# Kernel tuning notes

Measured on AMD Instinct MI355X. Metric: run time of the kernel, lower is better.

The kernel has to match this reference:

```python
import jax, jax.numpy as jnp
import numpy as np

GROUPS = 32
EPS = 1e-3  # keras GroupNormalization default epsilon


def setup_inputs() -> dict:
    key = jax.random.key(0)
    ks = jax.random.split(key, 7)
    B, H, W, C = 16, 32, 32, 512
    inputs = jax.random.normal(ks[0], (B, H, W, C), dtype=jnp.float32)
    gamma = jnp.ones((C,), dtype=jnp.float32)
    beta = jnp.zeros((C,), dtype=jnp.float32)
    # EinsumDense 'bhwc,cae->bhwae', output last dims (C,3), bias axes 'ae'
    W_qkv = jax.random.normal(ks[1], (C, C, 3), dtype=jnp.float32) / np.sqrt(C)
    b_qkv = jnp.zeros((C, 3), dtype=jnp.float32)
    # EinsumDense 'bhwc,cd->bhwd', bias axes 'd'
    W_out = jax.random.normal(ks[2], (C, C), dtype=jnp.float32) / np.sqrt(C)
    b_out = jnp.zeros((C,), dtype=jnp.float32)
    return {
        "inputs": inputs,
        "gamma": gamma,
        "beta": beta,
        "W_qkv": W_qkv,
        "b_qkv": b_qkv,
        "W_out": W_out,
        "b_out": b_out,
    }


def group_norm(x, gamma, beta):
    B, H, W, C = x.shape
    g = GROUPS
    xr = x.reshape(B, H, W, g, C // g)
    mean = jnp.mean(xr, axis=(1, 2, 4), keepdims=True)
    var = jnp.var(xr, axis=(1, 2, 4), keepdims=True)
    xn = (xr - mean) * jax.lax.rsqrt(var + EPS)
    return xn.reshape(B, H, W, C) * gamma + beta


def reference(inputs, gamma, beta, W_qkv, b_qkv, W_out, b_out):
    B, H, W, C = inputs.shape
    scale = C ** (-0.5)
    x = group_norm(inputs, gamma, beta)
    # QKV projection: bhwc,cae->bhwae  (+ bias over 'ae')
    qkv = jnp.einsum("bhwc,cae->bhwae", x, W_qkv) + b_qkv
    q, k, v = qkv[..., 0], qkv[..., 1], qkv[..., 2]  # each [B,H,W,C]
    # full spatial attention: [B,H,W,H,W]
    attn = jnp.einsum("bhwc,btlc->bhwtl", q, k) * scale
    attn = attn.reshape(B, H, W, H * W)
    attn = jax.nn.softmax(attn, axis=-1)
    attn = attn.reshape(B, H, W, H, W)
    out = jnp.einsum("bhwtl,btlc->bhwc", attn, v)
    out = jnp.einsum("bhwc,cd->bhwd", out, W_out) + b_out
    return inputs + out
```

## Files before the change

kernel.cpp:

```cpp
#include <hip/hip_runtime.h>
#include <hip/hip_bf16.h>

#define NB    16
#define SP    1024
#define NC    512
#define NG    32
#define MTOT  (NB*SP)
#define EPSV  1e-3f
#define SCALE 0.04419417382415922f

using f32x4   = __attribute__((ext_vector_type(4))) float;
using short8  = __attribute__((ext_vector_type(8))) short;
using short4v = __attribute__((ext_vector_type(4))) short;
using bf16x8v = __attribute__((ext_vector_type(8))) __bf16;

__device__ __forceinline__ unsigned short f2bf(float f) {
  union { float f; unsigned int u; } x; x.f = f;
  unsigned int u = x.u;
  unsigned int r = (u + 0x7FFFu + ((u >> 16) & 1u)) >> 16;
  return (unsigned short)r;
}

__global__ __launch_bounds__(256) void gn_stats_k(const float* __restrict__ x,
                                                  float2* __restrict__ stats) {
  int bg = blockIdx.x;
  int b = bg >> 5, g = bg & 31;
  int tid = threadIdx.x;
  int c = tid & 15, s0 = tid >> 4;
  const float* base = x + (long)b * SP * NC + g * 16 + c;
  float s = 0.f, ss = 0.f;
  for (int sp = s0; sp < SP; sp += 16) {
    float v = base[(long)sp * NC];
    s += v; ss += v * v;
  }
  for (int o = 32; o > 0; o >>= 1) { s += __shfl_xor(s, o); ss += __shfl_xor(ss, o); }
  __shared__ float rs[4], rss[4];
  int lane = tid & 63, wv = tid >> 6;
  if (lane == 0) { rs[wv] = s; rss[wv] = ss; }
  __syncthreads();
  if (tid == 0) {
    float S = rs[0] + rs[1] + rs[2] + rs[3];
    float SS = rss[0] + rss[1] + rss[2] + rss[3];
    float mean = S * (1.f / 16384.f);
    float var  = SS * (1.f / 16384.f) - mean * mean;
    stats[bg] = make_float2(mean, rsqrtf(var + EPSV));
  }
}

__global__ __launch_bounds__(256) void pack_wqkv_k(const float* __restrict__ W,
                                                   const float* __restrict__ bq,
                                                   unsigned short* __restrict__ Wp,
                                                   float* __restrict__ bp) {
  int idx = blockIdx.x * 256 + threadIdx.x;
  int n = idx >> 9, c = idx & 511;
  int e = n >> 9, a = n & 511;
  Wp[idx] = f2bf(W[((long)c * 512 + a) * 3 + e]);
  if (idx < 1536) {
    int e2 = idx >> 9, a2 = idx & 511;
    bp[idx] = bq[a2 * 3 + e2];
  }
}

__global__ __launch_bounds__(256) void pack_wout_k(const float* __restrict__ W,
                                                   unsigned short* __restrict__ Wp) {
  int idx = blockIdx.x * 256 + threadIdx.x;
  int n = idx >> 9, c = idx & 511;
  Wp[idx] = f2bf(W[(long)c * 512 + n]);
}

__global__ void transpose_v_k(const unsigned short* __restrict__ qkv,
                              unsigned short* __restrict__ vT) {
  __shared__ unsigned short t[32][33];
  int bs = blockIdx.x, bc = blockIdx.y, b = blockIdx.z;
  int tx = threadIdx.x, ty = threadIdx.y;
  #pragma unroll
  for (int k = 0; k < 4; ++k) {
    int s = bs * 32 + ty + k * 8, c = bc * 32 + tx;
    t[ty + k * 8][tx] = qkv[((long)b * SP + s) * 1536 + 1024 + c];
  }
  __syncthreads();
  #pragma unroll
  for (int k = 0; k < 4; ++k) {
    int c = bc * 32 + ty + k * 8, s = bs * 32 + tx;
    vT[((long)b * NC + c) * SP + s] = t[tx][ty + k * 8];
  }
}

__global__ __launch_bounds__(256) void softmax_k(float* __restrict__ S) {
  long row = blockIdx.x;
  const float* r = S + row * 1024;
  int tid = threadIdx.x, lane = tid & 63, wv = tid >> 6;
  f32x4 v = *reinterpret_cast<const f32x4*>(r + tid * 4);
  float m = fmaxf(fmaxf(v[0], v[1]), fmaxf(v[2], v[3]));
  for (int o = 32; o > 0; o >>= 1) m = fmaxf(m, __shfl_xor(m, o));
  __shared__ float wm[4], ws[4];
  if (lane == 0) wm[wv] = m;
  __syncthreads();
  float rmax = fmaxf(fmaxf(wm[0], wm[1]), fmaxf(wm[2], wm[3]));
  float e[4]; float ssum = 0.f;
  #pragma unroll
  for (int q = 0; q < 4; ++q) { e[q] = __expf(v[q] - rmax); ssum += e[q]; }
  for (int o = 32; o > 0; o >>= 1) ssum += __shfl_xor(ssum, o);
  if (lane == 0) ws[wv] = ssum;
  __syncthreads();
  float inv = 1.f / (ws[0] + ws[1] + ws[2] + ws[3]);
  short4v pv;
  #pragma unroll
  for (int q = 0; q < 4; ++q) pv[q] = (short)f2bf(e[q] * inv);
  unsigned short* P = reinterpret_cast<unsigned short*>(S);
  *reinterpret_cast<short4v*>(&P[row * 2048 + tid * 4]) = pv;
}

template <int AMODE, int EPI>
__global__ __launch_bounds__(256) void gemm_tn(
    const void* __restrict__ Apv, long strideA, int lda,
    const unsigned short* __restrict__ Bp, long strideB, int ldb,
    void* __restrict__ Op, long strideO, int ldo,
    const float* __restrict__ bias, const float* __restrict__ residual,
    const float2* __restrict__ stats,
    const float* __restrict__ gamma, const float* __restrict__ beta,
    int M, int N, int K, float scale) {
  __shared__ unsigned short As[128 * 72];
  __shared__ unsigned short Bs[128 * 72];
  const int tid = threadIdx.x;
  const int bm = blockIdx.y * 128, bn = blockIdx.x * 128;
  const int z = blockIdx.z;
  const int lane = tid & 63, wv = tid >> 6;
  const int wm = (wv >> 1) * 64, wn = (wv & 1) * 64;
  const int lrow = lane & 15, lk = (lane >> 4) * 8;
  const unsigned short* Bg = Bp + (long)z * strideB;

  f32x4 acc[4][4] = {};
  for (int kt = 0; kt < K; kt += 32) {
    #pragma unroll
    for (int it = 0; it < 2; ++it) {
      int cch = tid + it * 256;
      int row = cch >> 2, k8 = (cch & 3) << 3;
      *reinterpret_cast<short8*>(&Bs[row * 72 + k8]) =
          *reinterpret_cast<const short8*>(Bg + (long)(bn + row) * ldb + kt + k8);
    }
    if (AMODE == 0) {
      const unsigned short* Ag = (const unsigned short*)Apv + (long)z * strideA;
      #pragma unroll
      for (int it = 0; it < 2; ++it) {
        int cch = tid + it * 256;
        int row = cch >> 2, k8 = (cch & 3) << 3;
        *reinterpret_cast<short8*>(&As[row * 72 + k8]) =
            *reinterpret_cast<const short8*>(Ag + (long)(bm + row) * lda + kt + k8);
      }
    } else {
      const float* Xg = (const float*)Apv + (long)z * strideA;
      #pragma unroll
      for (int it = 0; it < 4; ++it) {
        int cch = tid + it * 256;
        int row = cch >> 3, col = (cch & 7) << 2;
        int rg = bm + row, ch = kt + col;
        f32x4 v  = *reinterpret_cast<const f32x4*>(Xg + (long)rg * lda + ch);
        f32x4 gm = *reinterpret_cast<const f32x4*>(gamma + ch);
        f32x4 bt = *reinterpret_cast<const f32x4*>(beta + ch);
        float2 st = stats[(rg >> 10) * NG + (ch >> 4)];
        short4v pv;
        #pragma unroll
        for (int q = 0; q < 4; ++q) {
          float sc = st.y * gm[q];
          pv[q] = (short)f2bf(v[q] * sc + (bt[q] - st.x * sc));
        }
        *reinterpret_cast<short4v*>(&As[row * 72 + col]) = pv;
      }
    }
    __syncthreads();
    short8 afr[4], bfr[4];
    #pragma unroll
    for (int i = 0; i < 4; ++i)
      afr[i] = *reinterpret_cast<const short8*>(&As[(wm + i * 16 + lrow) * 72 + lk]);
    #pragma unroll
    for (int j = 0; j < 4; ++j)
      bfr[j] = *reinterpret_cast<const short8*>(&Bs[(wn + j * 16 + lrow) * 72 + lk]);
    #pragma unroll
    for (int i = 0; i < 4; ++i)
      #pragma unroll
      for (int j = 0; j < 4; ++j)
        acc[i][j] = __builtin_amdgcn_mfma_f32_16x16x32_bf16(
            __builtin_bit_cast(bf16x8v, afr[i]),
            __builtin_bit_cast(bf16x8v, bfr[j]), acc[i][j], 0, 0, 0);
    __syncthreads();
  }

  const int colb = bn + wn + (lane & 15);
  #pragma unroll
  for (int i = 0; i < 4; ++i) {
    #pragma unroll
    for (int r = 0; r < 4; ++r) {
      int rowg = bm + wm + i * 16 + (lane >> 4) * 4 + r;
      #pragma unroll
      for (int j = 0; j < 4; ++j) {
        int colg = colb + j * 16;
        float v = acc[i][j][r];
        if (EPI == 0) {
          v += bias[colg];
          ((unsigned short*)Op)[(long)z * strideO + (long)rowg * ldo + colg] = f2bf(v);
        } else if (EPI == 1) {
          ((float*)Op)[(long)z * strideO + (long)rowg * ldo + colg] = v * scale;
        } else if (EPI == 2) {
          ((unsigned short*)Op)[(long)z * strideO + (long)rowg * ldo + colg] = f2bf(v);
        } else {
          v += bias[colg] + residual[(long)rowg * ldo + colg];
          ((float*)Op)[(long)rowg * ldo + colg] = v;
        }
      }
    }
  }
}

extern "C" void kernel_launch(void* const* d_in, const int* in_sizes, int n_in,
                              void* d_out, int out_size, void* d_ws, size_t ws_size,
                              hipStream_t stream) {
  const float* x     = (const float*)d_in[0];
  const float* gamma = (const float*)d_in[1];
  const float* beta  = (const float*)d_in[2];
  const float* Wqkv  = (const float*)d_in[3];
  const float* bqkv  = (const float*)d_in[4];
  const float* Wout  = (const float*)d_in[5];
  const float* bout  = (const float*)d_in[6];
  float* out = (float*)d_out;

  char* ws = (char*)d_ws;
  float2*         stats = (float2*)(ws + 0);
  unsigned short* wqkvP = (unsigned short*)(ws + 4096);
  float*          bqP   = (float*)(ws + 1576960);
  unsigned short* woutT = (unsigned short*)(ws + 1583104);
  unsigned short* qkv   = (unsigned short*)(ws + 2107392);
  unsigned short* vT    = (unsigned short*)(ws + 52439040);
  float*          Sbuf  = (float*)(ws + 69216256);
  unsigned short* attn  = (unsigned short*)(ws + 136325120);

  gn_stats_k<<<512, 256, 0, stream>>>(x, stats);
  pack_wqkv_k<<<3072, 256, 0, stream>>>(Wqkv, bqkv, wqkvP, bqP);
  pack_wout_k<<<1024, 256, 0, stream>>>(Wout, woutT);

  gemm_tn<1, 0><<<dim3(12, 128, 1), 256, 0, stream>>>(
      x, 0L, NC, wqkvP, 0L, NC, qkv, 0L, 1536,
      bqP, nullptr, stats, gamma, beta, MTOT, 1536, NC, 1.f);

  transpose_v_k<<<dim3(32, 16, 16), dim3(32, 8), 0, stream>>>(qkv, vT);

  gemm_tn<0, 1><<<dim3(8, 8, 16), 256, 0, stream>>>(
      qkv, (long)SP * 1536, 1536, qkv + 512, (long)SP * 1536, 1536,
      Sbuf, (long)SP * SP, SP, nullptr, nullptr, nullptr, nullptr, nullptr,
      SP, SP, NC, SCALE);

  softmax_k<<<MTOT, 256, 0, stream>>>(Sbuf);

  gemm_tn<0, 2><<<dim3(4, 8, 16), 256, 0, stream>>>(
      Sbuf, (long)SP * 2048, 2048, vT, (long)NC * SP, SP,
      attn, (long)SP * NC, NC, nullptr, nullptr, nullptr, nullptr, nullptr,
      SP, NC, SP, 1.f);

  gemm_tn<0, 3><<<dim3(4, 128, 1), 256, 0, stream>>>(
      attn, 0L, NC, woutT, 0L, NC, out, 0L, NC,
      bout, x, nullptr, nullptr, nullptr, MTOT, NC, NC, 1.f);
}
```

Measured before the change: 321.4 us.

## Use direct global-to-LDS loads in GEMM and split GroupNorm apply into own kernel

Replaces the register-staged tile loads in the shared GEMM with global_load_lds direct-to-LDS transfers into an unpadded 32-wide layout. Since the fused GroupNorm prologue in the QKV GEMM cannot use that path, a separate gn_apply kernel now writes a bf16 normalized copy of the input. This is meant to cut VGPR use and load-instruction overhead in every GEMM, at the cost of an extra pass over the input and losing the LDS row padding, which may raise bank conflicts on fragment reads.

Measured after the change: 299.7 us. 1.07x faster.

```diff
diff --git a/kernel.cpp b/kernel.cpp
--- a/kernel.cpp
+++ b/kernel.cpp
@@ -20,6 +20,11 @@
   unsigned int r = (u + 0x7FFFu + ((u >> 16) & 1u)) >> 16;
   return (unsigned short)r;
 }
+
+#define GLOAD_LDS16(g, l)                                                     \
+  __builtin_amdgcn_global_load_lds(                                           \
+      (const __attribute__((address_space(1))) void*)(g),                     \
+      (__attribute__((address_space(3))) void*)(l), 16, 0, 0)
 
 __global__ __launch_bounds__(256) void gn_stats_k(const float* __restrict__ x,
                                                   float2* __restrict__ stats) {
@@ -47,6 +52,36 @@
   }
 }
 
+__global__ __launch_bounds__(256) void gn_apply_k(const float* __restrict__ x,
+                                                  const float2* __restrict__ stats,
+                                                  const float* __restrict__ gamma,
+                                                  const float* __restrict__ beta,
+                                                  unsigned short* __restrict__ xn) {
+  long t = (long)blockIdx.x * 256 + threadIdx.x;
+  long base = t * 8;
+  int c = (int)(base & 511);
+  int b = (int)(base >> 19);
+  float2 st = stats[b * NG + (c >> 4)];
+  f32x4 v0 = *reinterpret_cast<const f32x4*>(x + base);
+  f32x4 v1 = *reinterpret_cast<const f32x4*>(x + base + 4);
+  f32x4 g0 = *reinterpret_cast<const f32x4*>(gamma + c);
+  f32x4 g1 = *reinterpret_cast<const f32x4*>(gamma + c + 4);
+  f32x4 b0 = *reinterpret_cast<const f32x4*>(beta + c);
+  f32x4 b1 = *reinterpret_cast<const f32x4*>(beta + c + 4);
+  short8 o;
+  #pragma unroll
+  for (int q = 0; q < 4; ++q) {
+    float sc = st.y * g0[q];
+    o[q] = (short)f2bf(v0[q] * sc + (b0[q] - st.x * sc));
+  }
+  #pragma unroll
+  for (int q = 0; q < 4; ++q) {
+    float sc = st.y * g1[q];
+    o[q + 4] = (short)f2bf(v1[q] * sc + (b1[q] - st.x * sc));
+  }
+  *reinterpret_cast<short8*>(xn + base) = o;
+}
+
 __global__ __launch_bounds__(256) void pack_wqkv_k(const float* __restrict__ W,
                                                    const float* __restrict__ bq,
                                                    unsigned short* __restrict__ Wp,
@@ -111,71 +146,45 @@
   *reinterpret_cast<short4v*>(&P[row * 2048 + tid * 4]) = pv;
 }
 
-template <int AMODE, int EPI>
+template <int EPI>
 __global__ __launch_bounds__(256) void gemm_tn(
-    const void* __restrict__ Apv, long strideA, int lda,
+    const unsigned short* __restrict__ Ap, long strideA, int lda,
     const unsigned short* __restrict__ Bp, long strideB, int ldb,
     void* __restrict__ Op, long strideO, int ldo,
     const float* __restrict__ bias, const float* __restrict__ residual,
-    const float2* __restrict__ stats,
-    const float* __restrict__ gamma, const float* __restrict__ beta,
-    int M, int N, int K, float scale) {
-  __shared__ unsigned short As[128 * 72];
-  __shared__ unsigned short Bs[128 * 72];
+    int K, float scale) {
+  __shared__ unsigned short As[128 * 32];
+  __shared__ unsigned short Bs[128 * 32];
   const int tid = threadIdx.x;
+  const int lane = tid & 63, wv = tid >> 6;
   const int bm = blockIdx.y * 128, bn = blockIdx.x * 128;
   const int z = blockIdx.z;
-  const int lane = tid & 63, wv = tid >> 6;
+  const unsigned short* Ag = Ap + (long)z * strideA;
+  const unsigned short* Bg = Bp + (long)z * strideB;
+
+  const int srow = lane >> 2;
+  const int scol = (lane & 3) * 8;
   const int wm = (wv >> 1) * 64, wn = (wv & 1) * 64;
   const int lrow = lane & 15, lk = (lane >> 4) * 8;
-  const unsigned short* Bg = Bp + (long)z * strideB;
 
   f32x4 acc[4][4] = {};
   for (int kt = 0; kt < K; kt += 32) {
     #pragma unroll
     for (int it = 0; it < 2; ++it) {
-      int cch = tid + it * 256;
-      int row = cch >> 2, k8 = (cch & 3) << 3;
-      *reinterpret_cast<short8*>(&Bs[row * 72 + k8]) =
-          *reinterpret_cast<const short8*>(Bg + (long)(bn + row) * ldb + kt + k8);
-    }
-    if (AMODE == 0) {
-      const unsigned short* Ag = (const unsigned short*)Apv + (long)z * strideA;
-      #pragma unroll
-      for (int it = 0; it < 2; ++it) {
-        int cch = tid + it * 256;
-        int row = cch >> 2, k8 = (cch & 3) << 3;
-        *reinterpret_cast<short8*>(&As[row * 72 + k8]) =
-            *reinterpret_cast<const short8*>(Ag + (long)(bm + row) * lda + kt + k8);
-      }
-    } else {
-      const float* Xg = (const float*)Apv + (long)z * strideA;
-      #pragma unroll
-      for (int it = 0; it < 4; ++it) {
-        int cch = tid + it * 256;
-        int row = cch >> 3, col = (cch & 7) << 2;
-        int rg = bm + row, ch = kt + col;
-        f32x4 v  = *reinterpret_cast<const f32x4*>(Xg + (long)rg * lda + ch);
-        f32x4 gm = *reinterpret_cast<const f32x4*>(gamma + ch);
-        f32x4 bt = *reinterpret_cast<const f32x4*>(beta + ch);
-        float2 st = stats[(rg >> 10) * NG + (ch >> 4)];
-        short4v pv;
-        #pragma unroll
-        for (int q = 0; q < 4; ++q) {
-          float sc = st.y * gm[q];
-          pv[q] = (short)f2bf(v[q] * sc + (bt[q] - st.x * sc));
-        }
-        *reinterpret_cast<short4v*>(&As[row * 72 + col]) = pv;
-      }
+      int chunk = it * 4 + wv;
+      int row = chunk * 16 + srow;
+      GLOAD_LDS16(Ag + (long)(bm + row) * lda + kt + scol, As + chunk * 512);
+      GLOAD_LDS16(Bg + (long)(bn + row) * ldb + kt + scol, Bs + chunk * 512);
     }
     __syncthreads();
+
     short8 afr[4], bfr[4];
     #pragma unroll
     for (int i = 0; i < 4; ++i)
-      afr[i] = *reinterpret_cast<const short8*>(&As[(wm + i * 16 + lrow) * 72 + lk]);
+      afr[i] = *reinterpret_cast<const short8*>(&As[(wm + i * 16 + lrow) * 32 + lk]);
     #pragma unroll
     for (int j = 0; j < 4; ++j)
-      bfr[j] = *reinterpret_cast<const short8*>(&Bs[(wn + j * 16 + lrow) * 72 + lk]);
+      bfr[j] = *reinterpret_cast<const short8*>(&Bs[(wn + j * 16 + lrow) * 32 + lk]);
     #pragma unroll
     for (int i = 0; i < 4; ++i)
       #pragma unroll
@@ -233,30 +242,30 @@
   unsigned short* vT    = (unsigned short*)(ws + 52439040);
   float*          Sbuf  = (float*)(ws + 69216256);
   unsigned short* attn  = (unsigned short*)(ws + 136325120);
+  unsigned short* xn    = (unsigned short*)(ws + 153102336);
 
   gn_stats_k<<<512, 256, 0, stream>>>(x, stats);
+  gn_apply_k<<<4096, 256, 0, stream>>>(x, stats, gamma, beta, xn);
   pack_wqkv_k<<<3072, 256, 0, stream>>>(Wqkv, bqkv, wqkvP, bqP);
   pack_wout_k<<<1024, 256, 0, stream>>>(Wout, woutT);
 
-  gemm_tn<1, 0><<<dim3(12, 128, 1), 256, 0, stream>>>(
-      x, 0L, NC, wqkvP, 0L, NC, qkv, 0L, 1536,
-      bqP, nullptr, stats, gamma, beta, MTOT, 1536, NC, 1.f);
+  gemm_tn<0><<<dim3(12, 128, 1), 256, 0, stream>>>(
+      xn, 0L, NC, wqkvP, 0L, NC, qkv, 0L, 1536,
+      bqP, nullptr, NC, 1.f);
 
   transpose_v_k<<<dim3(32, 16, 16), dim3(32, 8), 0, stream>>>(qkv, vT);
 
-  gemm_tn<0, 1><<<dim3(8, 8, 16), 256, 0, stream>>>(
+  gemm_tn<1><<<dim3(8, 8, 16), 256, 0, stream>>>(
       qkv, (long)SP * 1536, 1536, qkv + 512, (long)SP * 1536, 1536,
-      Sbuf, (long)SP * SP, SP, nullptr, nullptr, nullptr, nullptr, nullptr,
-      SP, SP, NC, SCALE);
+      Sbuf, (long)SP * SP, SP, nullptr, nullptr, NC, SCALE);
 
   softmax_k<<<MTOT, 256, 0, stream>>>(Sbuf);
 
-  gemm_tn<0, 2><<<dim3(4, 8, 16), 256, 0, stream>>>(
-      Sbuf, (long)SP * 2048, 2048, vT, (long)NC * SP, SP,
-      attn, (long)SP * NC, NC, nullptr, nullptr, nullptr, nullptr, nullptr,
-      SP, NC, SP, 1.f);
-
-  gemm_tn<0, 3><<<dim3(4, 128, 1), 256, 0, stream>>>(
+  gemm_tn<2><<<dim3(4, 8, 16), 256, 0, stream>>>(
+      (const unsigned short*)Sbuf, (long)SP * 2048, 2048, vT, (long)NC * SP, SP,
+      attn, (long)SP * NC, NC, nullptr, nullptr, SP, 1.f);
+
+  gemm_tn<3><<<dim3(4, 128, 1), 256, 0, stream>>>(
       attn, 0L, NC, woutT, 0L, NC, out, 0L, NC,
-      bout, x, nullptr, nullptr, nullptr, MTOT, NC, NC, 1.f);
-}
+      bout, x, NC, 1.f);
+}
```
